# Kernel optimization log

Measured on AMD Instinct MI355X. Metric: run time of the kernel, lower is better.

## Reference

```python
import jax, jax.numpy as jnp
import numpy as np

N, T, C, O, K, L = 10000, 8, 16, 64, 16, 3


def setup_inputs():
    key = jax.random.key(0)
    ks = jax.random.split(key, 8)
    s = 0.05
    return dict(
        X=jax.random.normal(ks[0], (N, T, C), jnp.float32),
        As=jax.random.randint(ks[1], (L, T, N, K), 0, N, dtype=jnp.int32),
        key_out=jnp.zeros((1,), jnp.float32),
        key_states=jnp.zeros((2, 1), jnp.float32),
        conv_w=jax.random.normal(ks[2], (L, O, C), jnp.float32) * s,
        conv_b=jax.random.normal(ks[3], (L, O), jnp.float32) * s,
        W_ih=jax.random.normal(ks[4], (L, 4 * O, O), jnp.float32) * s,
        W_hh=jax.random.normal(ks[5], (L, 4 * O, O), jnp.float32) * s,
        b_ih=jax.random.normal(ks[6], (L, 4 * O), jnp.float32) * s,
        b_hh=jax.random.normal(ks[7], (L, 4 * O), jnp.float32) * s,
    )


def _lstm(seq, W_ih, W_hh, b_ih, b_hh):
    # seq: [T, N, O]; PyTorch LSTM gate order i, f, g, o; zero initial state.
    H = W_hh.shape[1]
    n = seq.shape[1]

    def step(carry, xt):
        h, c = carry
        gates = xt @ W_ih.T + h @ W_hh.T + (b_ih + b_hh)
        i, f, g, o = jnp.split(gates, 4, axis=-1)
        c = jax.nn.sigmoid(f) * c + jax.nn.sigmoid(i) * jnp.tanh(g)
        h = jax.nn.sigmoid(o) * jnp.tanh(c)
        return (h, c), h

    init = (jnp.zeros((n, H), seq.dtype), jnp.zeros((n, H), seq.dtype))
    (h, c), ys = jax.lax.scan(step, init, seq)
    return ys, h, c


def _level(x, A, conv_w, conv_b, W_ih, W_hh, b_ih, b_hh):
    # x: [N,T,C], A: [T,N,K] neighbor indices (align=1: ego-subtract)
    xt = jnp.transpose(x, (1, 0, 2))                       # [T,N,C]
    gathered = jax.vmap(lambda xtt, At: xtt[At])(xt, A)    # [T,N,K,C]
    rel = gathered - xt[:, :, None, :]                     # [T,N,K,C]
    # 1x1 conv over channel dim + bias
    feat = jnp.einsum('tnkc,oc->tnko', rel, conv_w) + conv_b  # [T,N,K,O]
    feat = feat.max(axis=2)                                # max-pool over K -> [T,N,O]
    ys, h, c = _lstm(feat, W_ih, W_hh, b_ih, b_hh)         # ys [T,N,O]
    return ys, h, c


def reference(X, As, key_out, key_states, conv_w, conv_b, W_ih, W_hh, b_ih, b_hh):
    # key_out/key_states only used by attention aggregator (type 5); unused here.
    ys, h, c = jax.vmap(_level, in_axes=(None, 0, 0, 0, 0, 0, 0, 0))(
        X, As, conv_w, conv_b, W_ih, W_hh, b_ih, b_hh)     # ys [L,T,N,O], h/c [L,N,O]
    # level_aggregate_type=1: AdaptiveMaxPool2d over the level axis = max over L
    X_out = jnp.transpose(ys.max(axis=0), (1, 0, 2))       # [N,T,O]
    state_h = h.max(axis=0)[:, None, :]                    # [N,1,O]
    state_c = c.max(axis=0)[:, None, :]                    # [N,1,O]
    return X_out, state_h, state_c
```

## Files before the change

kernel.cpp:

```cpp
#include <hip/hip_runtime.h>
#include <hip/hip_bf16.h>

#define NN 10000
#define TT 8
#define LL 3
#define NGRP 625

typedef __bf16 bf16;
typedef __attribute__((ext_vector_type(8))) __bf16 bf16x8;
typedef __attribute__((ext_vector_type(4))) float f32x4;
typedef __attribute__((ext_vector_type(16))) float f32x16;

__device__ __forceinline__ float sigf(float x) {
    return __builtin_amdgcn_rcpf(1.0f + __expf(-x));
}
__device__ __forceinline__ float tanhf_(float x) {
    return fmaf(2.0f, __builtin_amdgcn_rcpf(1.0f + __expf(-2.0f * x)), -1.0f);
}

__global__ void prep_kernel(const float* __restrict__ W_ih, const float* __restrict__ W_hh,
                            const float* __restrict__ b_ih, const float* __restrict__ b_hh,
                            bf16* __restrict__ wts, float* __restrict__ bias) {
    int id = blockIdx.x * 256 + threadIdx.x;
    if (id < LL * 2 * 256 * 64) {
        int col = id & 63;
        int row = (id >> 6) & 255;
        int mat = (id >> 14) & 1;
        int l = id >> 15;
        const float* src = mat ? W_hh : W_ih;
        float w = src[(l * 256 + row) * 64 + col];
        int kh = col >> 5, nt = row >> 4, nn = row & 15, kk = col & 31;
        wts[((((l * 2 + mat) * 2 + kh) * 16 + nt) * 16 + nn) * 32 + kk] = (bf16)w;
    } else {
        int id2 = id - LL * 2 * 256 * 64;
        if (id2 < LL * 256) bias[id2] = b_ih[id2] + b_hh[id2];
    }
}

__global__ __launch_bounds__(256, 3) void fused_kernel(
    const float* __restrict__ X, const int* __restrict__ As,
    const float* __restrict__ conv_w, const float* __restrict__ conv_b,
    const bf16* __restrict__ wts, const float* __restrict__ bias,
    float* __restrict__ out) {
    __shared__ __align__(16) bf16 featL[TT][16][72];
    __shared__ __align__(16) bf16 hlds[2][16][72];

    const int tid = threadIdx.x;
    const int lane = tid & 63;
    const int wv = tid >> 6;
    const int c16 = lane & 15;
    const int q = lane >> 4;
    const int m = lane & 31;
    const int hh = lane >> 5;
    const int ch0 = hh * 8;
    const int nsub = m >> 4;
    const int kn = m & 15;
    const int node0 = blockIdx.x * 16;

    float ymax[TT][4];
#pragma unroll
    for (int t = 0; t < TT; ++t)
#pragma unroll
        for (int r = 0; r < 4; ++r) ymax[t][r] = -3.0e38f;
    float hfin[4], cfin[4];
#pragma unroll
    for (int r = 0; r < 4; ++r) { hfin[r] = -3.0e38f; cfin[r] = -3.0e38f; }

    for (int l = 0; l < LL; ++l) {
        __syncthreads();

        bf16x8 B0, B1;
        {
            const float* w0 = conv_w + ((l * 64 + m) * 16 + ch0);
            f32x4 a = *(const f32x4*)w0, b = *(const f32x4*)(w0 + 4);
            const float* w1 = conv_w + ((l * 64 + 32 + m) * 16 + ch0);
            f32x4 c = *(const f32x4*)w1, d = *(const f32x4*)(w1 + 4);
#pragma unroll
            for (int j = 0; j < 4; ++j) {
                B0[j] = (bf16)a[j]; B0[4 + j] = (bf16)b[j];
                B1[j] = (bf16)c[j]; B1[4 + j] = (bf16)d[j];
            }
        }
        const float cb0 = conv_b[l * 64 + m];
        const float cb1 = conv_b[l * 64 + 32 + m];

#pragma unroll 1
        for (int c = 0; c < 4; ++c) {
            const int pc = 2 * wv + (c & 1);
            const int t0 = (c >> 1) * 4;
            const int gn = node0 + 2 * pc + nsub;

            int aidx[4];
#pragma unroll
            for (int j = 0; j < 4; ++j)
                aidx[j] = As[((long)(l * 8 + t0 + j) * NN + gn) * 16 + kn];
            f32x4 sv[4][2], gv[4][2];
#pragma unroll
            for (int j = 0; j < 4; ++j) {
                const float* sp = X + ((gn * 8 + t0 + j) * 16 + ch0);
                sv[j][0] = *(const f32x4*)sp;
                sv[j][1] = *(const f32x4*)(sp + 4);
            }
#pragma unroll
            for (int j = 0; j < 4; ++j) {
                const float* gp = X + (((long)aidx[j] * 8 + t0 + j) * 16 + ch0);
                gv[j][0] = *(const f32x4*)gp;
                gv[j][1] = *(const f32x4*)(gp + 4);
            }

#pragma unroll
            for (int j = 0; j < 4; ++j) {
                bf16x8 af;
#pragma unroll
                for (int k = 0; k < 4; ++k) {
                    af[k]     = (bf16)(gv[j][0][k] - sv[j][0][k]);
                    af[4 + k] = (bf16)(gv[j][1][k] - sv[j][1][k]);
                }
                f32x16 D0, D1;
#pragma unroll
                for (int k = 0; k < 16; ++k) { D0[k] = 0.0f; D1[k] = 0.0f; }
                D0 = __builtin_amdgcn_mfma_f32_32x32x16_bf16(af, B0, D0, 0, 0, 0);
                D1 = __builtin_amdgcn_mfma_f32_32x32x16_bf16(af, B1, D1, 0, 0, 0);

                float v00 = D0[0], v01 = D1[0], v10 = D0[8], v11 = D1[8];
#pragma unroll
                for (int k = 1; k < 8; ++k) {
                    v00 = fmaxf(v00, D0[k]);     v01 = fmaxf(v01, D1[k]);
                    v10 = fmaxf(v10, D0[8 + k]); v11 = fmaxf(v11, D1[8 + k]);
                }
                v00 = fmaxf(v00, __shfl_xor(v00, 32));
                v01 = fmaxf(v01, __shfl_xor(v01, 32));
                v10 = fmaxf(v10, __shfl_xor(v10, 32));
                v11 = fmaxf(v11, __shfl_xor(v11, 32));

                const float sA = hh ? v10 : v00;
                const float sB = hh ? v11 : v01;
                featL[t0 + j][2 * pc + hh][m]      = (bf16)(sA + cb0);
                featL[t0 + j][2 * pc + hh][32 + m] = (bf16)(sB + cb1);
            }
        }

        const bf16* wb = wts + l * 32768;
        const int fo = c16 * 32 + q * 8;
        bf16x8 Bx0[4], Bx1[4], Bh0[4], Bh1[4];
        float brg[4];
#pragma unroll
        for (int g = 0; g < 4; ++g) {
            const int nt = 4 * g + wv;
            Bx0[g] = *(const bf16x8*)(wb + (0 * 16 + nt) * 512 + fo);
            Bx1[g] = *(const bf16x8*)(wb + (1 * 16 + nt) * 512 + fo);
            Bh0[g] = *(const bf16x8*)(wb + (2 * 16 + nt) * 512 + fo);
            Bh1[g] = *(const bf16x8*)(wb + (3 * 16 + nt) * 512 + fo);
            brg[g] = bias[l * 256 + nt * 16 + c16];
        }
        float c_r[4];
#pragma unroll
        for (int r = 0; r < 4; ++r) c_r[r] = 0.0f;

#pragma unroll
        for (int t = 0; t < TT; ++t) {
            __syncthreads();

            bf16x8 ax0 = *(const bf16x8*)&featL[t][c16][q * 8];
            bf16x8 ax1 = *(const bf16x8*)&featL[t][c16][32 + q * 8];
            bf16x8 ah0, ah1;
            if (t > 0) {
                ah0 = *(const bf16x8*)&hlds[(t + 1) & 1][c16][q * 8];
                ah1 = *(const bf16x8*)&hlds[(t + 1) & 1][c16][32 + q * 8];
            }

            f32x4 acc[4];
#pragma unroll
            for (int g = 0; g < 4; ++g) {
                float b = brg[g];
                acc[g] = (f32x4){b, b, b, b};
                acc[g] = __builtin_amdgcn_mfma_f32_16x16x32_bf16(ax0, Bx0[g], acc[g], 0, 0, 0);
                acc[g] = __builtin_amdgcn_mfma_f32_16x16x32_bf16(ax1, Bx1[g], acc[g], 0, 0, 0);
                if (t > 0) {
                    acc[g] = __builtin_amdgcn_mfma_f32_16x16x32_bf16(ah0, Bh0[g], acc[g], 0, 0, 0);
                    acc[g] = __builtin_amdgcn_mfma_f32_16x16x32_bf16(ah1, Bh1[g], acc[g], 0, 0, 0);
                }
            }

#pragma unroll
            for (int r = 0; r < 4; ++r) {
                float iv = acc[0][r], fv = acc[1][r], gg = acc[2][r], ov = acc[3][r];
                float c = sigf(fv) * c_r[r] + sigf(iv) * tanhf_(gg);
                c_r[r] = c;
                float h = sigf(ov) * tanhf_(c);
                hlds[t & 1][q * 4 + r][wv * 16 + c16] = (bf16)h;
                ymax[t][r] = fmaxf(ymax[t][r], h);
                if (t == TT - 1) {
                    hfin[r] = fmaxf(hfin[r], h);
                    cfin[r] = fmaxf(cfin[r], c);
                }
            }
        }
    }

    const int col = wv * 16 + c16;
#pragma unroll
    for (int t = 0; t < TT; ++t)
#pragma unroll
        for (int r = 0; r < 4; ++r)
            out[((long)(node0 + q * 4 + r) * 8 + t) * 64 + col] = ymax[t][r];
    float* sh = out + (long)NN * 8 * 64;
    float* sc = sh + (long)NN * 64;
#pragma unroll
    for (int r = 0; r < 4; ++r) {
        sh[(long)(node0 + q * 4 + r) * 64 + col] = hfin[r];
        sc[(long)(node0 + q * 4 + r) * 64 + col] = cfin[r];
    }
}

extern "C" void kernel_launch(void* const* d_in, const int* in_sizes, int n_in,
                              void* d_out, int out_size, void* d_ws, size_t ws_size,
                              hipStream_t stream) {
    const float* X = (const float*)d_in[0];
    const int* As = (const int*)d_in[1];
    const float* conv_w = (const float*)d_in[4];
    const float* conv_b = (const float*)d_in[5];
    const float* W_ih = (const float*)d_in[6];
    const float* W_hh = (const float*)d_in[7];
    const float* b_ih = (const float*)d_in[8];
    const float* b_hh = (const float*)d_in[9];
    float* out = (float*)d_out;

    char* ws = (char*)d_ws;
    bf16* wts = (bf16*)ws;
    float* bias = (float*)(ws + 196608);

    hipLaunchKernelGGL(prep_kernel, dim3(387), dim3(256), 0, stream,
                       W_ih, W_hh, b_ih, b_hh, wts, bias);
    hipLaunchKernelGGL(fused_kernel, dim3(NGRP), dim3(256), 0, stream,
                       X, As, conv_w, conv_b, wts, bias, out);
}
```

Before: 175.2 us.

## Split levels across blocks and reduce per-level slabs in separate kernel

Each block now handles one level for a group of 16 nodes instead of looping over all three levels serially, which triples the grid and lets the levels' recurrent LSTM chains run concurrently. Every level writes its outputs to its own workspace slab, and a new reduce kernel takes the elementwise max over the three slabs. This adds about 77 MB of slab writes plus reading them back, and one more kernel launch. The split path runs only if the workspace is large enough; otherwise the original fused kernel is used.

Measured after the change: 166.9 us. -4.8%, faster.

```diff
diff --git a/kernel.cpp b/kernel.cpp
--- a/kernel.cpp
+++ b/kernel.cpp
@@ -5,6 +5,10 @@
 #define TT 8
 #define LL 3
 #define NGRP 625
+
+#define OUT_ELEMS 6400000
+#define H_OFF 5120000
+#define C_OFF 5760000
 
 typedef __bf16 bf16;
 typedef __attribute__((ext_vector_type(8))) __bf16 bf16x8;
@@ -37,15 +41,13 @@
     }
 }
 
-__global__ __launch_bounds__(256, 3) void fused_kernel(
+__device__ __forceinline__ void level_body(
+    int l, int node0, int tid,
     const float* __restrict__ X, const int* __restrict__ As,
     const float* __restrict__ conv_w, const float* __restrict__ conv_b,
     const bf16* __restrict__ wts, const float* __restrict__ bias,
-    float* __restrict__ out) {
-    __shared__ __align__(16) bf16 featL[TT][16][72];
-    __shared__ __align__(16) bf16 hlds[2][16][72];
-
-    const int tid = threadIdx.x;
+    bf16 (*featL)[16][72], bf16 (*hlds)[16][72],
+    float ymax[TT][4], float hfin[4], float cfin[4], bool accum) {
     const int lane = tid & 63;
     const int wv = tid >> 6;
     const int c16 = lane & 15;
@@ -55,157 +57,213 @@
     const int ch0 = hh * 8;
     const int nsub = m >> 4;
     const int kn = m & 15;
+
+    bf16x8 B0, B1;
+    {
+        const float* w0 = conv_w + ((l * 64 + m) * 16 + ch0);
+        f32x4 a = *(const f32x4*)w0, b = *(const f32x4*)(w0 + 4);
+        const float* w1 = conv_w + ((l * 64 + 32 + m) * 16 + ch0);
+        f32x4 c = *(const f32x4*)w1, d = *(const f32x4*)(w1 + 4);
+#pragma unroll
+        for (int j = 0; j < 4; ++j) {
+            B0[j] = (bf16)a[j]; B0[4 + j] = (bf16)b[j];
+            B1[j] = (bf16)c[j]; B1[4 + j] = (bf16)d[j];
+        }
+    }
+    const float cb0 = conv_b[l * 64 + m];
+    const float cb1 = conv_b[l * 64 + 32 + m];
+
+#pragma unroll 1
+    for (int c = 0; c < 4; ++c) {
+        const int pc = 2 * wv + (c & 1);
+        const int t0 = (c >> 1) * 4;
+        const int gn = node0 + 2 * pc + nsub;
+
+        int aidx[4];
+#pragma unroll
+        for (int j = 0; j < 4; ++j)
+            aidx[j] = As[((long)(l * 8 + t0 + j) * NN + gn) * 16 + kn];
+        f32x4 sv[4][2], gv[4][2];
+#pragma unroll
+        for (int j = 0; j < 4; ++j) {
+            const float* sp = X + ((gn * 8 + t0 + j) * 16 + ch0);
+            sv[j][0] = *(const f32x4*)sp;
+            sv[j][1] = *(const f32x4*)(sp + 4);
+        }
+#pragma unroll
+        for (int j = 0; j < 4; ++j) {
+            const float* gp = X + (((long)aidx[j] * 8 + t0 + j) * 16 + ch0);
+            gv[j][0] = *(const f32x4*)gp;
+            gv[j][1] = *(const f32x4*)(gp + 4);
+        }
+
+#pragma unroll
+        for (int j = 0; j < 4; ++j) {
+            bf16x8 af;
+#pragma unroll
+            for (int k = 0; k < 4; ++k) {
+                af[k]     = (bf16)(gv[j][0][k] - sv[j][0][k]);
+                af[4 + k] = (bf16)(gv[j][1][k] - sv[j][1][k]);
+            }
+            f32x16 D0, D1;
+#pragma unroll
+            for (int k = 0; k < 16; ++k) { D0[k] = 0.0f; D1[k] = 0.0f; }
+            D0 = __builtin_amdgcn_mfma_f32_32x32x16_bf16(af, B0, D0, 0, 0, 0);
+            D1 = __builtin_amdgcn_mfma_f32_32x32x16_bf16(af, B1, D1, 0, 0, 0);
+
+            float v00 = D0[0], v01 = D1[0], v10 = D0[8], v11 = D1[8];
+#pragma unroll
+            for (int k = 1; k < 8; ++k) {
+                v00 = fmaxf(v00, D0[k]);     v01 = fmaxf(v01, D1[k]);
+                v10 = fmaxf(v10, D0[8 + k]); v11 = fmaxf(v11, D1[8 + k]);
+            }
+            v00 = fmaxf(v00, __shfl_xor(v00, 32));
+            v01 = fmaxf(v01, __shfl_xor(v01, 32));
+            v10 = fmaxf(v10, __shfl_xor(v10, 32));
+            v11 = fmaxf(v11, __shfl_xor(v11, 32));
+
+            const float sA = hh ? v10 : v00;
+            const float sB = hh ? v11 : v01;
+            featL[t0 + j][2 * pc + hh][m]      = (bf16)(sA + cb0);
+            featL[t0 + j][2 * pc + hh][32 + m] = (bf16)(sB + cb1);
+        }
+    }
+
+    const bf16* wb = wts + l * 32768;
+    const int fo = c16 * 32 + q * 8;
+    bf16x8 Bx0[4], Bx1[4], Bh0[4], Bh1[4];
+    float brg[4];
+#pragma unroll
+    for (int g = 0; g < 4; ++g) {
+        const int nt = 4 * g + wv;
+        Bx0[g] = *(const bf16x8*)(wb + (0 * 16 + nt) * 512 + fo);
+        Bx1[g] = *(const bf16x8*)(wb + (1 * 16 + nt) * 512 + fo);
+        Bh0[g] = *(const bf16x8*)(wb + (2 * 16 + nt) * 512 + fo);
+        Bh1[g] = *(const bf16x8*)(wb + (3 * 16 + nt) * 512 + fo);
+        brg[g] = bias[l * 256 + nt * 16 + c16];
+    }
+    float c_r[4];
+#pragma unroll
+    for (int r = 0; r < 4; ++r) c_r[r] = 0.0f;
+
+#pragma unroll
+    for (int t = 0; t < TT; ++t) {
+        __syncthreads();
+
+        bf16x8 ax0 = *(const bf16x8*)&featL[t][c16][q * 8];
+        bf16x8 ax1 = *(const bf16x8*)&featL[t][c16][32 + q * 8];
+        bf16x8 ah0, ah1;
+        if (t > 0) {
+            ah0 = *(const bf16x8*)&hlds[(t + 1) & 1][c16][q * 8];
+            ah1 = *(const bf16x8*)&hlds[(t + 1) & 1][c16][32 + q * 8];
+        }
+
+        f32x4 acc[4];
+#pragma unroll
+        for (int g = 0; g < 4; ++g) {
+            float b = brg[g];
+            acc[g] = (f32x4){b, b, b, b};
+            acc[g] = __builtin_amdgcn_mfma_f32_16x16x32_bf16(ax0, Bx0[g], acc[g], 0, 0, 0);
+            acc[g] = __builtin_amdgcn_mfma_f32_16x16x32_bf16(ax1, Bx1[g], acc[g], 0, 0, 0);
+            if (t > 0) {
+                acc[g] = __builtin_amdgcn_mfma_f32_16x16x32_bf16(ah0, Bh0[g], acc[g], 0, 0, 0);
+                acc[g] = __builtin_amdgcn_mfma_f32_16x16x32_bf16(ah1, Bh1[g], acc[g], 0, 0, 0);
+            }
+        }
+
+#pragma unroll
+        for (int r = 0; r < 4; ++r) {
+            float iv = acc[0][r], fv = acc[1][r], gg = acc[2][r], ov = acc[3][r];
+            float c = sigf(fv) * c_r[r] + sigf(iv) * tanhf_(gg);
+            c_r[r] = c;
+            float h = sigf(ov) * tanhf_(c);
+            hlds[t & 1][q * 4 + r][wv * 16 + c16] = (bf16)h;
+            ymax[t][r] = accum ? fmaxf(ymax[t][r], h) : h;
+            if (t == TT - 1) {
+                hfin[r] = accum ? fmaxf(hfin[r], h) : h;
+                cfin[r] = accum ? fmaxf(cfin[r], c) : c;
+            }
+        }
+    }
+}
+
+__global__ __launch_bounds__(256, 3) void fused_split_kernel(
+    const float* __restrict__ X, const int* __restrict__ As,
+    const float* __restrict__ conv_w, const float* __restrict__ conv_b,
+    const bf16* __restrict__ wts, const float* __restrict__ bias,
+    float* __restrict__ slabs) {
+    __shared__ __align__(16) bf16 featL[TT][16][72];
+    __shared__ __align__(16) bf16 hlds[2][16][72];
+
+    const int tid = threadIdx.x;
+    const int l = blockIdx.x % 3;
+    const int grp = blockIdx.x / 3;
+    const int node0 = grp * 16;
+
+    float ymax[TT][4], hfin[4], cfin[4];
+    level_body(l, node0, tid, X, As, conv_w, conv_b, wts, bias,
+               featL, hlds, ymax, hfin, cfin, false);
+
+    float* slab = slabs + (long)l * OUT_ELEMS;
+    const int lane = tid & 63;
+    const int wv = tid >> 6;
+    const int c16 = lane & 15;
+    const int q = lane >> 4;
+    const int col = wv * 16 + c16;
+#pragma unroll
+    for (int t = 0; t < TT; ++t)
+#pragma unroll
+        for (int r = 0; r < 4; ++r)
+            slab[((long)(node0 + q * 4 + r) * 8 + t) * 64 + col] = ymax[t][r];
+#pragma unroll
+    for (int r = 0; r < 4; ++r) {
+        slab[H_OFF + (long)(node0 + q * 4 + r) * 64 + col] = hfin[r];
+        slab[C_OFF + (long)(node0 + q * 4 + r) * 64 + col] = cfin[r];
+    }
+}
+
+__global__ __launch_bounds__(256) void reduce_kernel(
+    const float* __restrict__ slabs, float* __restrict__ out) {
+    const long i = (long)blockIdx.x * 256 + threadIdx.x;
+    const f32x4* s0 = (const f32x4*)slabs;
+    const f32x4* s1 = (const f32x4*)(slabs + OUT_ELEMS);
+    const f32x4* s2 = (const f32x4*)(slabs + 2L * OUT_ELEMS);
+    f32x4 a = s0[i], b = s1[i], c = s2[i], d;
+#pragma unroll
+    for (int k = 0; k < 4; ++k) d[k] = fmaxf(fmaxf(a[k], b[k]), c[k]);
+    ((f32x4*)out)[i] = d;
+}
+
+__global__ __launch_bounds__(256, 3) void fused_kernel(
+    const float* __restrict__ X, const int* __restrict__ As,
+    const float* __restrict__ conv_w, const float* __restrict__ conv_b,
+    const bf16* __restrict__ wts, const float* __restrict__ bias,
+    float* __restrict__ out) {
+    __shared__ __align__(16) bf16 featL[TT][16][72];
+    __shared__ __align__(16) bf16 hlds[2][16][72];
+
+    const int tid = threadIdx.x;
     const int node0 = blockIdx.x * 16;
 
-    float ymax[TT][4];
-#pragma unroll
-    for (int t = 0; t < TT; ++t)
-#pragma unroll
-        for (int r = 0; r < 4; ++r) ymax[t][r] = -3.0e38f;
-    float hfin[4], cfin[4];
-#pragma unroll
-    for (int r = 0; r < 4; ++r) { hfin[r] = -3.0e38f; cfin[r] = -3.0e38f; }
-
+    float ymax[TT][4], hfin[4], cfin[4];
     for (int l = 0; l < LL; ++l) {
         __syncthreads();
-
-        bf16x8 B0, B1;
-        {
-            const float* w0 = conv_w + ((l * 64 + m) * 16 + ch0);
-            f32x4 a = *(const f32x4*)w0, b = *(const f32x4*)(w0 + 4);
-            const float* w1 = conv_w + ((l * 64 + 32 + m) * 16 + ch0);
-            f32x4 c = *(const f32x4*)w1, d = *(const f32x4*)(w1 + 4);
-#pragma unroll
-            for (int j = 0; j < 4; ++j) {
-                B0[j] = (bf16)a[j]; B0[4 + j] = (bf16)b[j];
-                B1[j] = (bf16)c[j]; B1[4 + j] = (bf16)d[j];
-            }
-        }
-        const float cb0 = conv_b[l * 64 + m];
-        const float cb1 = conv_b[l * 64 + 32 + m];
-
-#pragma unroll 1
-        for (int c = 0; c < 4; ++c) {
-            const int pc = 2 * wv + (c & 1);
-            const int t0 = (c >> 1) * 4;
-            const int gn = node0 + 2 * pc + nsub;
-
-            int aidx[4];
-#pragma unroll
-            for (int j = 0; j < 4; ++j)
-                aidx[j] = As[((long)(l * 8 + t0 + j) * NN + gn) * 16 + kn];
-            f32x4 sv[4][2], gv[4][2];
-#pragma unroll
-            for (int j = 0; j < 4; ++j) {
-                const float* sp = X + ((gn * 8 + t0 + j) * 16 + ch0);
-                sv[j][0] = *(const f32x4*)sp;
-                sv[j][1] = *(const f32x4*)(sp + 4);
-            }
-#pragma unroll
-            for (int j = 0; j < 4; ++j) {
-                const float* gp = X + (((long)aidx[j] * 8 + t0 + j) * 16 + ch0);
-                gv[j][0] = *(const f32x4*)gp;
-                gv[j][1] = *(const f32x4*)(gp + 4);
-            }
-
-#pragma unroll
-            for (int j = 0; j < 4; ++j) {
-                bf16x8 af;
-#pragma unroll
-                for (int k = 0; k < 4; ++k) {
-                    af[k]     = (bf16)(gv[j][0][k] - sv[j][0][k]);
-                    af[4 + k] = (bf16)(gv[j][1][k] - sv[j][1][k]);
-                }
-                f32x16 D0, D1;
-#pragma unroll
-                for (int k = 0; k < 16; ++k) { D0[k] = 0.0f; D1[k] = 0.0f; }
-                D0 = __builtin_amdgcn_mfma_f32_32x32x16_bf16(af, B0, D0, 0, 0, 0);
-                D1 = __builtin_amdgcn_mfma_f32_32x32x16_bf16(af, B1, D1, 0, 0, 0);
-
-                float v00 = D0[0], v01 = D1[0], v10 = D0[8], v11 = D1[8];
-#pragma unroll
-                for (int k = 1; k < 8; ++k) {
-                    v00 = fmaxf(v00, D0[k]);     v01 = fmaxf(v01, D1[k]);
-                    v10 = fmaxf(v10, D0[8 + k]); v11 = fmaxf(v11, D1[8 + k]);
-                }
-                v00 = fmaxf(v00, __shfl_xor(v00, 32));
-                v01 = fmaxf(v01, __shfl_xor(v01, 32));
-                v10 = fmaxf(v10, __shfl_xor(v10, 32));
-                v11 = fmaxf(v11, __shfl_xor(v11, 32));
-
-                const float sA = hh ? v10 : v00;
-                const float sB = hh ? v11 : v01;
-                featL[t0 + j][2 * pc + hh][m]      = (bf16)(sA + cb0);
-                featL[t0 + j][2 * pc + hh][32 + m] = (bf16)(sB + cb1);
-            }
-        }
-
-        const bf16* wb = wts + l * 32768;
-        const int fo = c16 * 32 + q * 8;
-        bf16x8 Bx0[4], Bx1[4], Bh0[4], Bh1[4];
-        float brg[4];
-#pragma unroll
-        for (int g = 0; g < 4; ++g) {
-            const int nt = 4 * g + wv;
-            Bx0[g] = *(const bf16x8*)(wb + (0 * 16 + nt) * 512 + fo);
-            Bx1[g] = *(const bf16x8*)(wb + (1 * 16 + nt) * 512 + fo);
-            Bh0[g] = *(const bf16x8*)(wb + (2 * 16 + nt) * 512 + fo);
-            Bh1[g] = *(const bf16x8*)(wb + (3 * 16 + nt) * 512 + fo);
-            brg[g] = bias[l * 256 + nt * 16 + c16];
-        }
-        float c_r[4];
-#pragma unroll
-        for (int r = 0; r < 4; ++r) c_r[r] = 0.0f;
-
-#pragma unroll
-        for (int t = 0; t < TT; ++t) {
-            __syncthreads();
-
-            bf16x8 ax0 = *(const bf16x8*)&featL[t][c16][q * 8];
-            bf16x8 ax1 = *(const bf16x8*)&featL[t][c16][32 + q * 8];
-            bf16x8 ah0, ah1;
-            if (t > 0) {
-                ah0 = *(const bf16x8*)&hlds[(t + 1) & 1][c16][q * 8];
-                ah1 = *(const bf16x8*)&hlds[(t + 1) & 1][c16][32 + q * 8];
-            }
-
-            f32x4 acc[4];
-#pragma unroll
-            for (int g = 0; g < 4; ++g) {
-                float b = brg[g];
-                acc[g] = (f32x4){b, b, b, b};
-                acc[g] = __builtin_amdgcn_mfma_f32_16x16x32_bf16(ax0, Bx0[g], acc[g], 0, 0, 0);
-                acc[g] = __builtin_amdgcn_mfma_f32_16x16x32_bf16(ax1, Bx1[g], acc[g], 0, 0, 0);
-                if (t > 0) {
-                    acc[g] = __builtin_amdgcn_mfma_f32_16x16x32_bf16(ah0, Bh0[g], acc[g], 0, 0, 0);
-                    acc[g] = __builtin_amdgcn_mfma_f32_16x16x32_bf16(ah1, Bh1[g], acc[g], 0, 0, 0);
-                }
-            }
-
-#pragma unroll
-            for (int r = 0; r < 4; ++r) {
-                float iv = acc[0][r], fv = acc[1][r], gg = acc[2][r], ov = acc[3][r];
-                float c = sigf(fv) * c_r[r] + sigf(iv) * tanhf_(gg);
-                c_r[r] = c;
-                float h = sigf(ov) * tanhf_(c);
-                hlds[t & 1][q * 4 + r][wv * 16 + c16] = (bf16)h;
-                ymax[t][r] = fmaxf(ymax[t][r], h);
-                if (t == TT - 1) {
-                    hfin[r] = fmaxf(hfin[r], h);
-                    cfin[r] = fmaxf(cfin[r], c);
-                }
-            }
-        }
-    }
-
+        level_body(l, node0, tid, X, As, conv_w, conv_b, wts, bias,
+                   featL, hlds, ymax, hfin, cfin, (l > 0));
+    }
+
+    const int lane = tid & 63;
+    const int wv = tid >> 6;
+    const int c16 = lane & 15;
+    const int q = lane >> 4;
     const int col = wv * 16 + c16;
 #pragma unroll
     for (int t = 0; t < TT; ++t)
 #pragma unroll
         for (int r = 0; r < 4; ++r)
             out[((long)(node0 + q * 4 + r) * 8 + t) * 64 + col] = ymax[t][r];
-    float* sh = out + (long)NN * 8 * 64;
-    float* sc = sh + (long)NN * 64;
+    float* sh = out + (long)H_OFF;
+    float* sc = out + (long)C_OFF;
 #pragma unroll
     for (int r = 0; r < 4; ++r) {
         sh[(long)(node0 + q * 4 + r) * 64 + col] = hfin[r];
@@ -227,11 +285,25 @@
     float* out = (float*)d_out;
 
     char* ws = (char*)d_ws;
-    bf16* wts = (bf16*)ws;
-    float* bias = (float*)(ws + 196608);
-
-    hipLaunchKernelGGL(prep_kernel, dim3(387), dim3(256), 0, stream,
-                       W_ih, W_hh, b_ih, b_hh, wts, bias);
-    hipLaunchKernelGGL(fused_kernel, dim3(NGRP), dim3(256), 0, stream,
-                       X, As, conv_w, conv_b, wts, bias, out);
-}
+    const size_t slabs_bytes = (size_t)3 * OUT_ELEMS * 4;
+    const bool big_ws = ws_size >= slabs_bytes + 196608 + 4096;
+
+    if (big_ws) {
+        float* slabs = (float*)ws;
+        bf16* wts = (bf16*)(ws + slabs_bytes);
+        float* bias = (float*)(ws + slabs_bytes + 196608);
+        hipLaunchKernelGGL(prep_kernel, dim3(387), dim3(256), 0, stream,
+                           W_ih, W_hh, b_ih, b_hh, wts, bias);
+        hipLaunchKernelGGL(fused_split_kernel, dim3(3 * NGRP), dim3(256), 0, stream,
+                           X, As, conv_w, conv_b, wts, bias, slabs);
+        hipLaunchKernelGGL(reduce_kernel, dim3(OUT_ELEMS / 4 / 256), dim3(256), 0, stream,
+                           slabs, out);
+    } else {
+        bf16* wts = (bf16*)ws;
+        float* bias = (float*)(ws + 196608);
+        hipLaunchKernelGGL(prep_kernel, dim3(387), dim3(256), 0, stream,
+                           W_ih, W_hh, b_ih, b_hh, wts, bias);
+        hipLaunchKernelGGL(fused_kernel, dim3(NGRP), dim3(256), 0, stream,
+                           X, As, conv_w, conv_b, wts, bias, out);
+    }
+}
```

## Split levels across blocks and combine outputs with atomic float max

Applied to the files above, without the earlier changes.

The fused kernel now launches one block per (node group, level) instead of looping over the three levels inside each block. That triples the grid from 625 to 1875 blocks so the GPU has more parallelism. Outputs are combined with a CAS-based atomic float max, so the prep kernel is enlarged to first fill the whole output with -inf. The cost is an extra full-output initialization write plus contended atomic CAS traffic on every output element, in exchange for better occupancy and latency hiding.

New measurement: 296.3 us. 1.69x slower.

```diff
diff --git a/kernel.cpp b/kernel.cpp
--- a/kernel.cpp
+++ b/kernel.cpp
@@ -6,6 +6,10 @@
 #define LL 3
 #define NGRP 625
 
+#define OUT_ELEMS 6400000
+#define H_OFF 5120000
+#define C_OFF 5760000
+
 typedef __bf16 bf16;
 typedef __attribute__((ext_vector_type(8))) __bf16 bf16x8;
 typedef __attribute__((ext_vector_type(4))) float f32x4;
@@ -18,10 +22,28 @@
     return fmaf(2.0f, __builtin_amdgcn_rcpf(1.0f + __expf(-2.0f * x)), -1.0f);
 }
 
-__global__ void prep_kernel(const float* __restrict__ W_ih, const float* __restrict__ W_hh,
-                            const float* __restrict__ b_ih, const float* __restrict__ b_hh,
-                            bf16* __restrict__ wts, float* __restrict__ bias) {
-    int id = blockIdx.x * 256 + threadIdx.x;
+__device__ __forceinline__ void atomicFmax(float* addr, float val) {
+    unsigned* ua = (unsigned*)addr;
+    unsigned old = 0xFF800000u;
+    const unsigned vbits = __float_as_uint(val);
+    while (true) {
+        const unsigned assumed = old;
+        old = atomicCAS(ua, assumed, vbits);
+        if (old == assumed) break;
+        if (__uint_as_float(old) >= val) break;
+    }
+}
+
+__global__ __launch_bounds__(256) void prep_init_kernel(
+    const float* __restrict__ W_ih, const float* __restrict__ W_hh,
+    const float* __restrict__ b_ih, const float* __restrict__ b_hh,
+    bf16* __restrict__ wts, float* __restrict__ bias,
+    float* __restrict__ out) {
+    const int id = blockIdx.x * 256 + threadIdx.x;
+
+    const float ninf = __uint_as_float(0xFF800000u);
+    ((f32x4*)out)[id] = (f32x4){ninf, ninf, ninf, ninf};
+
     if (id < LL * 2 * 256 * 64) {
         int col = id & 63;
         int row = (id >> 6) & 255;
@@ -31,13 +53,13 @@
         float w = src[(l * 256 + row) * 64 + col];
         int kh = col >> 5, nt = row >> 4, nn = row & 15, kk = col & 31;
         wts[((((l * 2 + mat) * 2 + kh) * 16 + nt) * 16 + nn) * 32 + kk] = (bf16)w;
-    } else {
+    } else if (id < LL * 2 * 256 * 64 + LL * 256) {
         int id2 = id - LL * 2 * 256 * 64;
-        if (id2 < LL * 256) bias[id2] = b_ih[id2] + b_hh[id2];
-    }
-}
-
-__global__ __launch_bounds__(256, 3) void fused_kernel(
+        bias[id2] = b_ih[id2] + b_hh[id2];
+    }
+}
+
+__global__ __launch_bounds__(256, 3) void fused_split_kernel(
     const float* __restrict__ X, const int* __restrict__ As,
     const float* __restrict__ conv_w, const float* __restrict__ conv_b,
     const bf16* __restrict__ wts, const float* __restrict__ bias,
@@ -46,6 +68,10 @@
     __shared__ __align__(16) bf16 hlds[2][16][72];
 
     const int tid = threadIdx.x;
+    const int l = blockIdx.x % 3;
+    const int grp = blockIdx.x / 3;
+    const int node0 = grp * 16;
+
     const int lane = tid & 63;
     const int wv = tid >> 6;
     const int c16 = lane & 15;
@@ -55,161 +81,147 @@
     const int ch0 = hh * 8;
     const int nsub = m >> 4;
     const int kn = m & 15;
-    const int node0 = blockIdx.x * 16;
-
-    float ymax[TT][4];
+
+    bf16x8 B0, B1;
+    {
+        const float* w0 = conv_w + ((l * 64 + m) * 16 + ch0);
+        f32x4 a = *(const f32x4*)w0, b = *(const f32x4*)(w0 + 4);
+        const float* w1 = conv_w + ((l * 64 + 32 + m) * 16 + ch0);
+        f32x4 c = *(const f32x4*)w1, d = *(const f32x4*)(w1 + 4);
+#pragma unroll
+        for (int j = 0; j < 4; ++j) {
+            B0[j] = (bf16)a[j]; B0[4 + j] = (bf16)b[j];
+            B1[j] = (bf16)c[j]; B1[4 + j] = (bf16)d[j];
+        }
+    }
+    const float cb0 = conv_b[l * 64 + m];
+    const float cb1 = conv_b[l * 64 + 32 + m];
+
+#pragma unroll 1
+    for (int c = 0; c < 4; ++c) {
+        const int pc = 2 * wv + (c & 1);
+        const int t0 = (c >> 1) * 4;
+        const int gn = node0 + 2 * pc + nsub;
+
+        int aidx[4];
+#pragma unroll
+        for (int j = 0; j < 4; ++j)
+            aidx[j] = As[((long)(l * 8 + t0 + j) * NN + gn) * 16 + kn];
+        f32x4 sv[4][2], gv[4][2];
+#pragma unroll
+        for (int j = 0; j < 4; ++j) {
+            const float* sp = X + ((gn * 8 + t0 + j) * 16 + ch0);
+            sv[j][0] = *(const f32x4*)sp;
+            sv[j][1] = *(const f32x4*)(sp + 4);
+        }
+#pragma unroll
+        for (int j = 0; j < 4; ++j) {
+            const float* gp = X + (((long)aidx[j] * 8 + t0 + j) * 16 + ch0);
+            gv[j][0] = *(const f32x4*)gp;
+            gv[j][1] = *(const f32x4*)(gp + 4);
+        }
+
+#pragma unroll
+        for (int j = 0; j < 4; ++j) {
+            bf16x8 af;
+#pragma unroll
+            for (int k = 0; k < 4; ++k) {
+                af[k]     = (bf16)(gv[j][0][k] - sv[j][0][k]);
+                af[4 + k] = (bf16)(gv[j][1][k] - sv[j][1][k]);
+            }
+            f32x16 D0, D1;
+#pragma unroll
+            for (int k = 0; k < 16; ++k) { D0[k] = 0.0f; D1[k] = 0.0f; }
+            D0 = __builtin_amdgcn_mfma_f32_32x32x16_bf16(af, B0, D0, 0, 0, 0);
+            D1 = __builtin_amdgcn_mfma_f32_32x32x16_bf16(af, B1, D1, 0, 0, 0);
+
+            float v00 = D0[0], v01 = D1[0], v10 = D0[8], v11 = D1[8];
+#pragma unroll
+            for (int k = 1; k < 8; ++k) {
+                v00 = fmaxf(v00, D0[k]);     v01 = fmaxf(v01, D1[k]);
+                v10 = fmaxf(v10, D0[8 + k]); v11 = fmaxf(v11, D1[8 + k]);
+            }
+            v00 = fmaxf(v00, __shfl_xor(v00, 32));
+            v01 = fmaxf(v01, __shfl_xor(v01, 32));
+            v10 = fmaxf(v10, __shfl_xor(v10, 32));
+            v11 = fmaxf(v11, __shfl_xor(v11, 32));
+
+            const float sA = hh ? v10 : v00;
+            const float sB = hh ? v11 : v01;
+            featL[t0 + j][2 * pc + hh][m]      = (bf16)(sA + cb0);
+            featL[t0 + j][2 * pc + hh][32 + m] = (bf16)(sB + cb1);
+        }
+    }
+
+    const bf16* wb = wts + l * 32768;
+    const int fo = c16 * 32 + q * 8;
+    bf16x8 Bx0[4], Bx1[4], Bh0[4], Bh1[4];
+    float brg[4];
+#pragma unroll
+    for (int g = 0; g < 4; ++g) {
+        const int nt = 4 * g + wv;
+        Bx0[g] = *(const bf16x8*)(wb + (0 * 16 + nt) * 512 + fo);
+        Bx1[g] = *(const bf16x8*)(wb + (1 * 16 + nt) * 512 + fo);
+        Bh0[g] = *(const bf16x8*)(wb + (2 * 16 + nt) * 512 + fo);
+        Bh1[g] = *(const bf16x8*)(wb + (3 * 16 + nt) * 512 + fo);
+        brg[g] = bias[l * 256 + nt * 16 + c16];
+    }
+    float c_r[4];
+#pragma unroll
+    for (int r = 0; r < 4; ++r) c_r[r] = 0.0f;
+
+    float ymax[TT][4], hfin[4], cfin[4];
+
+#pragma unroll
+    for (int t = 0; t < TT; ++t) {
+        __syncthreads();
+
+        bf16x8 ax0 = *(const bf16x8*)&featL[t][c16][q * 8];
+        bf16x8 ax1 = *(const bf16x8*)&featL[t][c16][32 + q * 8];
+        bf16x8 ah0, ah1;
+        if (t > 0) {
+            ah0 = *(const bf16x8*)&hlds[(t + 1) & 1][c16][q * 8];
+            ah1 = *(const bf16x8*)&hlds[(t + 1) & 1][c16][32 + q * 8];
+        }
+
+        f32x4 acc[4];
+#pragma unroll
+        for (int g = 0; g < 4; ++g) {
+            float b = brg[g];
+            acc[g] = (f32x4){b, b, b, b};
+            acc[g] = __builtin_amdgcn_mfma_f32_16x16x32_bf16(ax0, Bx0[g], acc[g], 0, 0, 0);
+            acc[g] = __builtin_amdgcn_mfma_f32_16x16x32_bf16(ax1, Bx1[g], acc[g], 0, 0, 0);
+            if (t > 0) {
+                acc[g] = __builtin_amdgcn_mfma_f32_16x16x32_bf16(ah0, Bh0[g], acc[g], 0, 0, 0);
+                acc[g] = __builtin_amdgcn_mfma_f32_16x16x32_bf16(ah1, Bh1[g], acc[g], 0, 0, 0);
+            }
+        }
+
+#pragma unroll
+        for (int r = 0; r < 4; ++r) {
+            float iv = acc[0][r], fv = acc[1][r], gg = acc[2][r], ov = acc[3][r];
+            float c = sigf(fv) * c_r[r] + sigf(iv) * tanhf_(gg);
+            c_r[r] = c;
+            float h = sigf(ov) * tanhf_(c);
+            hlds[t & 1][q * 4 + r][wv * 16 + c16] = (bf16)h;
+            ymax[t][r] = h;
+            if (t == TT - 1) { hfin[r] = h; cfin[r] = c; }
+        }
+    }
+
+    const int col = wv * 16 + c16;
 #pragma unroll
     for (int t = 0; t < TT; ++t)
 #pragma unroll
-        for (int r = 0; r < 4; ++r) ymax[t][r] = -3.0e38f;
-    float hfin[4], cfin[4];
-#pragma unroll
-    for (int r = 0; r < 4; ++r) { hfin[r] = -3.0e38f; cfin[r] = -3.0e38f; }
-
-    for (int l = 0; l < LL; ++l) {
-        __syncthreads();
-
-        bf16x8 B0, B1;
-        {
-            const float* w0 = conv_w + ((l * 64 + m) * 16 + ch0);
-            f32x4 a = *(const f32x4*)w0, b = *(const f32x4*)(w0 + 4);
-            const float* w1 = conv_w + ((l * 64 + 32 + m) * 16 + ch0);
-            f32x4 c = *(const f32x4*)w1, d = *(const f32x4*)(w1 + 4);
-#pragma unroll
-            for (int j = 0; j < 4; ++j) {
-                B0[j] = (bf16)a[j]; B0[4 + j] = (bf16)b[j];
-                B1[j] = (bf16)c[j]; B1[4 + j] = (bf16)d[j];
-            }
-        }
-        const float cb0 = conv_b[l * 64 + m];
-        const float cb1 = conv_b[l * 64 + 32 + m];
-
-#pragma unroll 1
-        for (int c = 0; c < 4; ++c) {
-            const int pc = 2 * wv + (c & 1);
-            const int t0 = (c >> 1) * 4;
-            const int gn = node0 + 2 * pc + nsub;
-
-            int aidx[4];
-#pragma unroll
-            for (int j = 0; j < 4; ++j)
-                aidx[j] = As[((long)(l * 8 + t0 + j) * NN + gn) * 16 + kn];
-            f32x4 sv[4][2], gv[4][2];
-#pragma unroll
-            for (int j = 0; j < 4; ++j) {
-                const float* sp = X + ((gn * 8 + t0 + j) * 16 + ch0);
-                sv[j][0] = *(const f32x4*)sp;
-                sv[j][1] = *(const f32x4*)(sp + 4);
-            }
-#pragma unroll
-            for (int j = 0; j < 4; ++j) {
-                const float* gp = X + (((long)aidx[j] * 8 + t0 + j) * 16 + ch0);
-                gv[j][0] = *(const f32x4*)gp;
-                gv[j][1] = *(const f32x4*)(gp + 4);
-            }
-
-#pragma unroll
-            for (int j = 0; j < 4; ++j) {
-                bf16x8 af;
-#pragma unroll
-                for (int k = 0; k < 4; ++k) {
-                    af[k]     = (bf16)(gv[j][0][k] - sv[j][0][k]);
-                    af[4 + k] = (bf16)(gv[j][1][k] - sv[j][1][k]);
-                }
-                f32x16 D0, D1;
-#pragma unroll
-                for (int k = 0; k < 16; ++k) { D0[k] = 0.0f; D1[k] = 0.0f; }
-                D0 = __builtin_amdgcn_mfma_f32_32x32x16_bf16(af, B0, D0, 0, 0, 0);
-                D1 = __builtin_amdgcn_mfma_f32_32x32x16_bf16(af, B1, D1, 0, 0, 0);
-
-                float v00 = D0[0], v01 = D1[0], v10 = D0[8], v11 = D1[8];
-#pragma unroll
-                for (int k = 1; k < 8; ++k) {
-                    v00 = fmaxf(v00, D0[k]);     v01 = fmaxf(v01, D1[k]);
-                    v10 = fmaxf(v10, D0[8 + k]); v11 = fmaxf(v11, D1[8 + k]);
-                }
-                v00 = fmaxf(v00, __shfl_xor(v00, 32));
-                v01 = fmaxf(v01, __shfl_xor(v01, 32));
-                v10 = fmaxf(v10, __shfl_xor(v10, 32));
-                v11 = fmaxf(v11, __shfl_xor(v11, 32));
-
-                const float sA = hh ? v10 : v00;
-                const float sB = hh ? v11 : v01;
-                featL[t0 + j][2 * pc + hh][m]      = (bf16)(sA + cb0);
-                featL[t0 + j][2 * pc + hh][32 + m] = (bf16)(sB + cb1);
-            }
-        }
-
-        const bf16* wb = wts + l * 32768;
-        const int fo = c16 * 32 + q * 8;
-        bf16x8 Bx0[4], Bx1[4], Bh0[4], Bh1[4];
-        float brg[4];
-#pragma unroll
-        for (int g = 0; g < 4; ++g) {
-            const int nt = 4 * g + wv;
-            Bx0[g] = *(const bf16x8*)(wb + (0 * 16 + nt) * 512 + fo);
-            Bx1[g] = *(const bf16x8*)(wb + (1 * 16 + nt) * 512 + fo);
-            Bh0[g] = *(const bf16x8*)(wb + (2 * 16 + nt) * 512 + fo);
-            Bh1[g] = *(const bf16x8*)(wb + (3 * 16 + nt) * 512 + fo);
-            brg[g] = bias[l * 256 + nt * 16 + c16];
-        }
-        float c_r[4];
-#pragma unroll
-        for (int r = 0; r < 4; ++r) c_r[r] = 0.0f;
-
-#pragma unroll
-        for (int t = 0; t < TT; ++t) {
-            __syncthreads();
-
-            bf16x8 ax0 = *(const bf16x8*)&featL[t][c16][q * 8];
-            bf16x8 ax1 = *(const bf16x8*)&featL[t][c16][32 + q * 8];
-            bf16x8 ah0, ah1;
-            if (t > 0) {
-                ah0 = *(const bf16x8*)&hlds[(t + 1) & 1][c16][q * 8];
-                ah1 = *(const bf16x8*)&hlds[(t + 1) & 1][c16][32 + q * 8];
-            }
-
-            f32x4 acc[4];
-#pragma unroll
-            for (int g = 0; g < 4; ++g) {
-                float b = brg[g];
-                acc[g] = (f32x4){b, b, b, b};
-                acc[g] = __builtin_amdgcn_mfma_f32_16x16x32_bf16(ax0, Bx0[g], acc[g], 0, 0, 0);
-                acc[g] = __builtin_amdgcn_mfma_f32_16x16x32_bf16(ax1, Bx1[g], acc[g], 0, 0, 0);
-                if (t > 0) {
-                    acc[g] = __builtin_amdgcn_mfma_f32_16x16x32_bf16(ah0, Bh0[g], acc[g], 0, 0, 0);
-                    acc[g] = __builtin_amdgcn_mfma_f32_16x16x32_bf16(ah1, Bh1[g], acc[g], 0, 0, 0);
-                }
-            }
-
-#pragma unroll
-            for (int r = 0; r < 4; ++r) {
-                float iv = acc[0][r], fv = acc[1][r], gg = acc[2][r], ov = acc[3][r];
-                float c = sigf(fv) * c_r[r] + sigf(iv) * tanhf_(gg);
-                c_r[r] = c;
-                float h = sigf(ov) * tanhf_(c);
-                hlds[t & 1][q * 4 + r][wv * 16 + c16] = (bf16)h;
-                ymax[t][r] = fmaxf(ymax[t][r], h);
-                if (t == TT - 1) {
-                    hfin[r] = fmaxf(hfin[r], h);
-                    cfin[r] = fmaxf(cfin[r], c);
-                }
-            }
-        }
-    }
-
-    const int col = wv * 16 + c16;
-#pragma unroll
-    for (int t = 0; t < TT; ++t)
-#pragma unroll
         for (int r = 0; r < 4; ++r)
-            out[((long)(node0 + q * 4 + r) * 8 + t) * 64 + col] = ymax[t][r];
-    float* sh = out + (long)NN * 8 * 64;
-    float* sc = sh + (long)NN * 64;
+            atomicFmax(&out[((long)(node0 + q * 4 + r) * 8 + t) * 64 + col],
+                       ymax[t][r]);
+    float* sh = out + (long)H_OFF;
+    float* sc = out + (long)C_OFF;
 #pragma unroll
     for (int r = 0; r < 4; ++r) {
-        sh[(long)(node0 + q * 4 + r) * 64 + col] = hfin[r];
-        sc[(long)(node0 + q * 4 + r) * 64 + col] = cfin[r];
+        atomicFmax(&sh[(long)(node0 + q * 4 + r) * 64 + col], hfin[r]);
+        atomicFmax(&sc[(long)(node0 + q * 4 + r) * 64 + col], cfin[r]);
     }
 }
 
@@ -230,8 +242,8 @@
     bf16* wts = (bf16*)ws;
     float* bias = (float*)(ws + 196608);
 
-    hipLaunchKernelGGL(prep_kernel, dim3(387), dim3(256), 0, stream,
-                       W_ih, W_hh, b_ih, b_hh, wts, bias);
-    hipLaunchKernelGGL(fused_kernel, dim3(NGRP), dim3(256), 0, stream,
+    hipLaunchKernelGGL(prep_init_kernel, dim3(6250), dim3(256), 0, stream,
+                       W_ih, W_hh, b_ih, b_hh, wts, bias, out);
+    hipLaunchKernelGGL(fused_split_kernel, dim3(3 * NGRP), dim3(256), 0, stream,
                        X, As, conv_w, conv_b, wts, bias, out);
 }
```
